# Optimization experiments

Measured on AMD Instinct MI355X. Metric: run time of the kernel, lower is better.

Reference implementation:

```python
import jax, jax.numpy as jnp
import numpy as np

N = 100000
D = 128      # embedding_dim
HID = 32     # hidden per head
HEADS = 4
OUT_C = 64
E = 1600000
NEG_SLOPE = 0.2


def setup_inputs() -> dict:
    key = jax.random.key(0)
    ks = jax.random.split(key, 12)
    inp = {}
    inp["x_indices"] = jnp.arange(N, dtype=jnp.int64)
    inp["ei"] = jax.random.randint(ks[0], (2, E), 0, N, dtype=jnp.int64)
    # parameters
    inp["emb"] = jax.random.normal(ks[1], (N, D), dtype=jnp.float32)
    # conv1: in=D, out=HID per head, HEADS heads, concat
    s1 = 1.0 / np.sqrt(D)
    inp["W1"] = jax.random.normal(ks[2], (D, HEADS * HID), dtype=jnp.float32) * s1
    inp["a_src1"] = jax.random.normal(ks[3], (HEADS, HID), dtype=jnp.float32) * s1
    inp["a_dst1"] = jax.random.normal(ks[4], (HEADS, HID), dtype=jnp.float32) * s1
    inp["b1"] = jnp.zeros((HEADS * HID,), dtype=jnp.float32)
    # conv2: in=HEADS*HID, out=OUT_C, 1 head
    s2 = 1.0 / np.sqrt(HEADS * HID)
    inp["W2"] = jax.random.normal(ks[5], (HEADS * HID, OUT_C), dtype=jnp.float32) * s2
    inp["a_src2"] = jax.random.normal(ks[6], (1, OUT_C), dtype=jnp.float32) * s2
    inp["a_dst2"] = jax.random.normal(ks[7], (1, OUT_C), dtype=jnp.float32) * s2
    inp["b2"] = jnp.zeros((OUT_C,), dtype=jnp.float32)
    return inp


def gat_conv(x, src, dst, W, a_src, a_dst, b, heads, out_ch, concat):
    # x: [N, Din]; src/dst: [E'] (self-loops already included)
    n = x.shape[0]
    h = (x @ W).reshape(n, heads, out_ch)          # [N, H, C]
    alpha_s = jnp.sum(h * a_src, axis=-1)          # [N, H]
    alpha_d = jnp.sum(h * a_dst, axis=-1)          # [N, H]
    e = alpha_s[src] + alpha_d[dst]                # [E', H]
    e = jnp.where(e > 0, e, NEG_SLOPE * e)         # leaky_relu
    # segment softmax over incoming edges per destination node
    m = jax.ops.segment_max(e, dst, num_segments=n)      # [N, H]
    ex = jnp.exp(e - m[dst])
    den = jax.ops.segment_sum(ex, dst, num_segments=n)   # [N, H]
    a = ex / den[dst]                              # [E', H]  (self-loops guarantee den>0)
    msg = h[src] * a[:, :, None]                   # [E', H, C]
    out = jax.ops.segment_sum(msg, dst, num_segments=n)  # [N, H, C]
    if concat:
        out = out.reshape(n, heads * out_ch)
    else:
        out = out.mean(axis=1)
    return out + b


def reference(x_indices, ei, emb, W1, a_src1, a_dst1, b1, W2, a_src2, a_dst2, b2):
    n = emb.shape[0]
    # PyG GATConv default add_self_loops=True
    loop = jnp.arange(n, dtype=ei.dtype)
    src = jnp.concatenate([ei[0], loop])
    dst = jnp.concatenate([ei[1], loop])
    x = emb[x_indices]                                  # embedding lookup
    x = jax.nn.elu(gat_conv(x, src, dst, W1, a_src1, a_dst1, b1, HEADS, HID, True))
    # dropout p=0.5 is identity in eval mode
    return gat_conv(x, src, dst, W2, a_src2, a_dst2, b2, 1, OUT_C, True)
```

## Files before the change

kernel.cpp:

```cpp
#include <hip/hip_runtime.h>
#include <math.h>

#define NEG_SLOPE 0.2f
#define BK_SHIFT 8

typedef __attribute__((ext_vector_type(2))) float v2f;

__device__ __forceinline__ float leaky(float x) { return x > 0.f ? x : NEG_SLOPE * x; }
__device__ __forceinline__ float dot4(float4 a, float4 b) {
    return a.x * b.x + a.y * b.y + a.z * b.z + a.w * b.w;
}
__device__ __forceinline__ unsigned short f2bf(float f) {
    unsigned int x = __float_as_uint(f);
    unsigned int r = (x + 0x7fffu + ((x >> 16) & 1u)) >> 16;
    return (unsigned short)r;
}
__device__ __forceinline__ float bflo(unsigned int u) { return __uint_as_float(u << 16); }
__device__ __forceinline__ float bfhi(unsigned int u) { return __uint_as_float(u & 0xffff0000u); }


__global__ void zero_kernel(int* __restrict__ p, int n) {
    int i = blockIdx.x * blockDim.x + threadIdx.x;
    if (i < n) p[i] = 0;
}

__global__ void __launch_bounds__(256) bcount_kernel(const int* __restrict__ ei, int E, int E2,
                                                     int K, int* __restrict__ bcounts) {
    __shared__ int h[512];
    int t = threadIdx.x;
    h[t] = 0; h[t + 256] = 0;
    __syncthreads();
    int base = blockIdx.x * 4096;
#pragma unroll 4
    for (int i = 0; i < 16; i++) {
        int e = base + i * 256 + t;
        if (e < E2) {
            int dst = (e < E) ? ei[E + e] : (e - E);
            atomicAdd(&h[dst >> BK_SHIFT], 1);
        }
    }
    __syncthreads();
    for (int b = t; b < K; b += 256) {
        int c = h[b];
        if (c) atomicAdd(&bcounts[b], c);
    }
}

__global__ void __launch_bounds__(512) bscan_kernel(const int* __restrict__ bcounts, int K,
                                                    int* __restrict__ bbase, int* __restrict__ bcursor) {
    __shared__ int s[512];
    int t = threadIdx.x;
    int v = (t < K) ? bcounts[t] : 0;
    s[t] = v;
    __syncthreads();
    for (int off = 1; off < 512; off <<= 1) {
        int u = (t >= off) ? s[t - off] : 0;
        __syncthreads();
        s[t] += u;
        __syncthreads();
    }
    if (t < K) {
        int ex = s[t] - v;
        bbase[t] = ex;
        bcursor[t] = ex;
    }
    if (t == 511) bbase[K] = s[511];
}

__global__ void __launch_bounds__(256) bscatter_kernel(const int* __restrict__ ei, int E, int E2,
                                                       int K, int* __restrict__ bcursor,
                                                       unsigned int* __restrict__ bedges) {
    __shared__ int hist[512], pre[512], lcur[512], gbase[512], psum[256];
    __shared__ unsigned int stage[4096];
    __shared__ unsigned short binof[4096];
    int t = threadIdx.x;
    hist[t] = 0; hist[t + 256] = 0;
    __syncthreads();
    int base = blockIdx.x * 4096;
    int cnt = min(4096, E2 - base);
    int s_[16], d_[16];
#pragma unroll
    for (int i = 0; i < 16; i++) {
        int e = base + i * 256 + t;
        if (e < E2) {
            int ss, dd;
            if (e < E) { ss = ei[e]; dd = ei[E + e]; }
            else       { ss = e - E; dd = ss; }
            s_[i] = ss; d_[i] = dd;
            atomicAdd(&hist[dd >> BK_SHIFT], 1);
        }
    }
    __syncthreads();
    int a0 = hist[2 * t], a1 = hist[2 * t + 1];
    psum[t] = a0 + a1;
    __syncthreads();
    for (int off = 1; off < 256; off <<= 1) {
        int u = (t >= off) ? psum[t - off] : 0;
        __syncthreads();
        psum[t] += u;
        __syncthreads();
    }
    int pex = psum[t] - (a0 + a1);
    pre[2 * t] = pex;
    pre[2 * t + 1] = pex + a0;
    __syncthreads();
    for (int b = t; b < K; b += 256) {
        int c = hist[b];
        if (c) gbase[b] = atomicAdd(&bcursor[b], c);
    }
    lcur[t] = pre[t]; lcur[t + 256] = pre[t + 256];
    __syncthreads();
#pragma unroll
    for (int i = 0; i < 16; i++) {
        int e = base + i * 256 + t;
        if (e < E2) {
            int bin = d_[i] >> BK_SHIFT;
            int p = atomicAdd(&lcur[bin], 1);
            stage[p] = ((unsigned)s_[i] << 8) | (unsigned)(d_[i] & 255);
            binof[p] = (unsigned short)bin;
        }
    }
    __syncthreads();
    for (int i = t; i < cnt; i += 256) {
        unsigned int ed = stage[i];
        int bin = (int)binof[i];
        bedges[gbase[bin] + (i - pre[bin])] = ed;
    }
}

__global__ void __launch_bounds__(256) bcsr_kernel(const unsigned int* __restrict__ bedges,
                                                   const int* __restrict__ bbase, int N,
                                                   int* __restrict__ counts, int* __restrict__ indptr,
                                                   int* __restrict__ csr) {
    __shared__ int hist[256], scn[256], cur[256];
    int b = blockIdx.x;
    int t = threadIdx.x;
    int base = bbase[b];
    int cnt = bbase[b + 1] - base;
    hist[t] = 0;
    __syncthreads();
    for (int i = t; i < cnt; i += 256) {
        atomicAdd(&hist[bedges[base + i] & 255u], 1);
    }
    __syncthreads();
    int v = hist[t];
    scn[t] = v;
    __syncthreads();
    for (int off = 1; off < 256; off <<= 1) {
        int u = (t >= off) ? scn[t - off] : 0;
        __syncthreads();
        scn[t] += u;
        __syncthreads();
    }
    int ex = scn[t] - v;
    int d = (b << BK_SHIFT) + t;
    if (d < N) { counts[d] = v; indptr[d] = base + ex; }
    cur[t] = ex;
    __syncthreads();
    for (int i = t; i < cnt; i += 256) {
        unsigned int ed = bedges[base + i];
        int p = atomicAdd(&cur[ed & 255u], 1);
        csr[base + p] = (int)(ed >> 8);
    }
}


__global__ __launch_bounds__(256) void gemm1_kernel(const float* __restrict__ emb,
                             const int* __restrict__ xidx,
                             const float* __restrict__ W1,
                             unsigned short* __restrict__ h1b,
                             const float* __restrict__ a_s1, const float* __restrict__ a_d1,
                             float* __restrict__ as1, float* __restrict__ ad1, int N) {
    __shared__ float xs[64][128];
    __shared__ float ws[128][64];
    int tid = threadIdx.x;
    int r0 = blockIdx.x * 64;
    int c0 = blockIdx.y * 64;
    {
        const float4* W4 = (const float4*)W1;
        float4* ws4 = (float4*)ws;
        int cbase = c0 >> 2;
        for (int i = tid; i < 128 * 16; i += 256) {
            int k = i >> 4, c = i & 15;
            ws4[i] = W4[k * 32 + cbase + c];
        }
    }
    {
        float4* xs4 = (float4*)xs;
        for (int i = tid; i < 64 * 32; i += 256) {
            int r = i >> 5, c = i & 31;
            int row = r0 + r;
            float4 v = make_float4(0.f, 0.f, 0.f, 0.f);
            if (row < N) {
                int s = xidx[row];
                v = ((const float4*)emb)[(size_t)s * 32 + c];
            }
            xs4[i] = v;
        }
    }
    __syncthreads();
    int tr = tid >> 4;
    int tc = tid & 15;
    float4 acc[4];
    acc[0] = acc[1] = acc[2] = acc[3] = make_float4(0.f, 0.f, 0.f, 0.f);
    for (int k = 0; k < 128; k += 4) {
        float4 wv0 = *(const float4*)&ws[k][tc * 4];
        float4 wv1 = *(const float4*)&ws[k + 1][tc * 4];
        float4 wv2 = *(const float4*)&ws[k + 2][tc * 4];
        float4 wv3 = *(const float4*)&ws[k + 3][tc * 4];
#pragma unroll
        for (int i = 0; i < 4; i++) {
            float4 xv = *(const float4*)&xs[tr * 4 + i][k];
            acc[i].x = fmaf(xv.x, wv0.x, acc[i].x);
            acc[i].y = fmaf(xv.x, wv0.y, acc[i].y);
            acc[i].z = fmaf(xv.x, wv0.z, acc[i].z);
            acc[i].w = fmaf(xv.x, wv0.w, acc[i].w);
            acc[i].x = fmaf(xv.y, wv1.x, acc[i].x);
            acc[i].y = fmaf(xv.y, wv1.y, acc[i].y);
            acc[i].z = fmaf(xv.y, wv1.z, acc[i].z);
            acc[i].w = fmaf(xv.y, wv1.w, acc[i].w);
            acc[i].x = fmaf(xv.z, wv2.x, acc[i].x);
            acc[i].y = fmaf(xv.z, wv2.y, acc[i].y);
            acc[i].z = fmaf(xv.z, wv2.z, acc[i].z);
            acc[i].w = fmaf(xv.z, wv2.w, acc[i].w);
            acc[i].x = fmaf(xv.w, wv3.x, acc[i].x);
            acc[i].y = fmaf(xv.w, wv3.y, acc[i].y);
            acc[i].z = fmaf(xv.w, wv3.z, acc[i].z);
            acc[i].w = fmaf(xv.w, wv3.w, acc[i].w);
        }
    }
    int colbase = c0 + tc * 4;
    int h = colbase >> 5;
    int off = colbase & 31;
    float4 av = *(const float4*)&a_s1[h * 32 + off];
    float4 dv = *(const float4*)&a_d1[h * 32 + off];
#pragma unroll
    for (int i = 0; i < 4; i++) {
        int row = r0 + tr * 4 + i;
        if (row < N) {
            ushort4 pk;
            pk.x = f2bf(acc[i].x); pk.y = f2bf(acc[i].y);
            pk.z = f2bf(acc[i].z); pk.w = f2bf(acc[i].w);
            *(ushort4*)&h1b[(size_t)row * 128 + colbase] = pk;
        }
        float ps = dot4(acc[i], av);
        float pd = dot4(acc[i], dv);
        ps += __shfl_xor(ps, 1); pd += __shfl_xor(pd, 1);
        ps += __shfl_xor(ps, 2); pd += __shfl_xor(pd, 2);
        ps += __shfl_xor(ps, 4); pd += __shfl_xor(pd, 4);
        if ((tc & 7) == 0 && row < N) {
            as1[row * 4 + h] = ps;
            ad1[row * 4 + h] = pd;
        }
    }
}


__global__ __launch_bounds__(256) void gemm2_kernel(const unsigned short* __restrict__ x1b,
                             const float* __restrict__ W2,
                             unsigned short* __restrict__ h2b,
                             const float* __restrict__ a_s2, const float* __restrict__ a_d2,
                             float* __restrict__ as2, float* __restrict__ ad2, int N) {
    __shared__ float xs[64][128];
    __shared__ float ws[128][64];
    int tid = threadIdx.x;
    int r0 = blockIdx.x * 64;
    {
        const float4* W4 = (const float4*)W2;
        float4* ws4 = (float4*)ws;
        for (int i = tid; i < 128 * 16; i += 256) ws4[i] = W4[i];
    }
    {
        const uint4* x4 = (const uint4*)x1b;
        for (int i = tid; i < 64 * 16; i += 256) {
            int r = i >> 4, c = i & 15;
            int row = r0 + r;
            uint4 u = make_uint4(0u, 0u, 0u, 0u);
            if (row < N) u = x4[(size_t)row * 16 + c];
            float* dst = &xs[r][c * 8];
            dst[0] = bflo(u.x); dst[1] = bfhi(u.x);
            dst[2] = bflo(u.y); dst[3] = bfhi(u.y);
            dst[4] = bflo(u.z); dst[5] = bfhi(u.z);
            dst[6] = bflo(u.w); dst[7] = bfhi(u.w);
        }
    }
    __syncthreads();
    int tr = tid >> 4;
    int tc = tid & 15;
    float4 acc[4];
    acc[0] = acc[1] = acc[2] = acc[3] = make_float4(0.f, 0.f, 0.f, 0.f);
    for (int k = 0; k < 128; k += 4) {
        float4 wv0 = *(const float4*)&ws[k][tc * 4];
        float4 wv1 = *(const float4*)&ws[k + 1][tc * 4];
        float4 wv2 = *(const float4*)&ws[k + 2][tc * 4];
        float4 wv3 = *(const float4*)&ws[k + 3][tc * 4];
#pragma unroll
        for (int i = 0; i < 4; i++) {
            float4 xv = *(const float4*)&xs[tr * 4 + i][k];
            acc[i].x = fmaf(xv.x, wv0.x, acc[i].x);
            acc[i].y = fmaf(xv.x, wv0.y, acc[i].y);
            acc[i].z = fmaf(xv.x, wv0.z, acc[i].z);
            acc[i].w = fmaf(xv.x, wv0.w, acc[i].w);
            acc[i].x = fmaf(xv.y, wv1.x, acc[i].x);
            acc[i].y = fmaf(xv.y, wv1.y, acc[i].y);
            acc[i].z = fmaf(xv.y, wv1.z, acc[i].z);
            acc[i].w = fmaf(xv.y, wv1.w, acc[i].w);
            acc[i].x = fmaf(xv.z, wv2.x, acc[i].x);
            acc[i].y = fmaf(xv.z, wv2.y, acc[i].y);
            acc[i].z = fmaf(xv.z, wv2.z, acc[i].z);
            acc[i].w = fmaf(xv.z, wv2.w, acc[i].w);
            acc[i].x = fmaf(xv.w, wv3.x, acc[i].x);
            acc[i].y = fmaf(xv.w, wv3.y, acc[i].y);
            acc[i].z = fmaf(xv.w, wv3.z, acc[i].z);
            acc[i].w = fmaf(xv.w, wv3.w, acc[i].w);
        }
    }
    float4 av = *(const float4*)&a_s2[tc * 4];
    float4 dv = *(const float4*)&a_d2[tc * 4];
#pragma unroll
    for (int i = 0; i < 4; i++) {
        int row = r0 + tr * 4 + i;
        if (row < N) {
            ushort4 pk;
            pk.x = f2bf(acc[i].x); pk.y = f2bf(acc[i].y);
            pk.z = f2bf(acc[i].z); pk.w = f2bf(acc[i].w);
            *(ushort4*)&h2b[(size_t)row * 64 + tc * 4] = pk;
        }
        float ps = dot4(acc[i], av);
        float pd = dot4(acc[i], dv);
        ps += __shfl_xor(ps, 1); pd += __shfl_xor(pd, 1);
        ps += __shfl_xor(ps, 2); pd += __shfl_xor(pd, 2);
        ps += __shfl_xor(ps, 4); pd += __shfl_xor(pd, 4);
        ps += __shfl_xor(ps, 8); pd += __shfl_xor(pd, 8);
        if (tc == 0 && row < N) { as2[row] = ps; ad2[row] = pd; }
    }
}


__device__ __forceinline__ void edge_fma(uint4 u0, float w, v2f* acc) {
    v2f wv = {w, w};
    v2f t;
    t.x = bflo(u0.x); t.y = bfhi(u0.x); acc[0] += wv * t;
    t.x = bflo(u0.y); t.y = bfhi(u0.y); acc[1] += wv * t;
    t.x = bflo(u0.z); t.y = bfhi(u0.z); acc[2] += wv * t;
    t.x = bflo(u0.w); t.y = bfhi(u0.w); acc[3] += wv * t;
}

__device__ __forceinline__ void accum_tbl1(int srcReg, const float* __restrict__ ew, int mcount,
                                           const uint4* __restrict__ h1v4,
                                           int lanebase, int sub, int cg, int hh, v2f* acc) {
    int b = 0;
    for (; b + 4 <= mcount; b += 4) {
        int i0 = b + sub, i1 = b + 2 + sub;
        int s0 = __shfl(srcReg, lanebase + i0);
        int s1 = __shfl(srcReg, lanebase + i1);
        float w_0 = ew[i0 * 4 + hh];
        float w_1 = ew[i1 * 4 + hh];
        uint4 u0 = h1v4[(unsigned)(s0 * 16 + cg)];
        uint4 u1 = h1v4[(unsigned)(s1 * 16 + cg)];
        edge_fma(u0, w_0, acc);
        edge_fma(u1, w_1, acc);
    }
    if (b + 2 <= mcount) {
        int i0 = b + sub;
        int s0 = __shfl(srcReg, lanebase + i0);
        float w_0 = ew[i0 * 4 + hh];
        uint4 u0 = h1v4[(unsigned)(s0 * 16 + cg)];
        edge_fma(u0, w_0, acc);
        b += 2;
    }
    if (b < mcount) {
        int s0 = __shfl(srcReg, lanebase + b);
        if (sub == 0) {
            float w_0 = ew[b * 4 + hh];
            uint4 u0 = h1v4[(unsigned)(s0 * 16 + cg)];
            edge_fma(u0, w_0, acc);
        }
    }
}

__global__ void __launch_bounds__(256)
agg1_kernel(const int* __restrict__ csr, const int* __restrict__ indptr,
            const int* __restrict__ counts, const float* __restrict__ as1,
            const float* __restrict__ ad1, const unsigned short* __restrict__ h1b,
            const float* __restrict__ b1, unsigned short* __restrict__ x1b, int N) {
    __shared__ float ewt[4][2][128];
    int lane = threadIdx.x & 63;
    int wv = threadIdx.x >> 6;
    int l32 = lane & 31;
    int lanebase = lane & 32;
    int n = blockIdx.x * 8 + wv * 2 + (lane >> 5);
    if (n >= N) return;
    int start = indptr[n];
    int cnt = counts[n];
    float4 ad4 = ((const float4*)ad1)[n];

    int src0 = 0;
    float4 p0 = make_float4(0.f, 0.f, 0.f, 0.f);
    if (l32 < cnt) {
        src0 = csr[start + l32];
        float4 a = ((const float4*)as1)[src0];
        p0.x = __expf(leaky(a.x + ad4.x));
        p0.y = __expf(leaky(a.y + ad4.y));
        p0.z = __expf(leaky(a.z + ad4.z));
        p0.w = __expf(leaky(a.w + ad4.w));
    }
    float4 l4 = p0;
    if (cnt > 32) {
        for (int base = 32; base < cnt; base += 32) {
            if (base + l32 < cnt) {
                int s = csr[start + base + l32];
                float4 a = ((const float4*)as1)[s];
                l4.x += __expf(leaky(a.x + ad4.x));
                l4.y += __expf(leaky(a.y + ad4.y));
                l4.z += __expf(leaky(a.z + ad4.z));
                l4.w += __expf(leaky(a.w + ad4.w));
            }
        }
    }
#pragma unroll
    for (int off = 16; off >= 1; off >>= 1) {
        l4.x += __shfl_xor(l4.x, off);
        l4.y += __shfl_xor(l4.y, off);
        l4.z += __shfl_xor(l4.z, off);
        l4.w += __shfl_xor(l4.w, off);
    }
    float4 li = make_float4(1.f / l4.x, 1.f / l4.y, 1.f / l4.z, 1.f / l4.w);
    float4 w0 = make_float4(p0.x * li.x, p0.y * li.y, p0.z * li.z, p0.w * li.w);

    float* ew = ewt[wv][lane >> 5];
    *(float4*)&ew[l32 * 4] = w0;

    int sub = l32 >> 4;
    int cg = lane & 15;
    int hh = cg >> 2;
    const uint4* h1v4 = (const uint4*)h1b;
    v2f acc[4];
    acc[0] = acc[1] = acc[2] = acc[3] = (v2f){0.f, 0.f};
    accum_tbl1(src0, ew, min(cnt, 32), h1v4, lanebase, sub, cg, hh, acc);
    if (cnt > 32) {
        for (int base = 32; base < cnt; base += 32) {
            int srcc = 0;
            float4 wc = make_float4(0.f, 0.f, 0.f, 0.f);
            if (base + l32 < cnt) {
                srcc = csr[start + base + l32];
                float4 a = ((const float4*)as1)[srcc];
                wc.x = __expf(leaky(a.x + ad4.x)) * li.x;
                wc.y = __expf(leaky(a.y + ad4.y)) * li.y;
                wc.z = __expf(leaky(a.z + ad4.z)) * li.z;
                wc.w = __expf(leaky(a.w + ad4.w)) * li.w;
            }
            *(float4*)&ew[l32 * 4] = wc;
            accum_tbl1(srcc, ew, min(cnt - base, 32), h1v4, lanebase, sub, cg, hh, acc);
        }
    }
#pragma unroll
    for (int i = 0; i < 4; i++) {
        acc[i].x += __shfl_xor(acc[i].x, 16);
        acc[i].y += __shfl_xor(acc[i].y, 16);
    }
    if (l32 < 16) {
        const float4* b4 = (const float4*)b1;
        float4 ba = b4[cg * 2], bb = b4[cg * 2 + 1];
        float o[8];
        o[0] = acc[0].x + ba.x; o[1] = acc[0].y + ba.y;
        o[2] = acc[1].x + ba.z; o[3] = acc[1].y + ba.w;
        o[4] = acc[2].x + bb.x; o[5] = acc[2].y + bb.y;
        o[6] = acc[3].x + bb.z; o[7] = acc[3].y + bb.w;
#pragma unroll
        for (int j = 0; j < 8; j++) o[j] = (o[j] > 0.f) ? o[j] : (__expf(o[j]) - 1.f);
        uint4 pk;
        pk.x = (unsigned)f2bf(o[0]) | ((unsigned)f2bf(o[1]) << 16);
        pk.y = (unsigned)f2bf(o[2]) | ((unsigned)f2bf(o[3]) << 16);
        pk.z = (unsigned)f2bf(o[4]) | ((unsigned)f2bf(o[5]) << 16);
        pk.w = (unsigned)f2bf(o[6]) | ((unsigned)f2bf(o[7]) << 16);
        *(uint4*)&x1b[(size_t)n * 128 + cg * 8] = pk;
    }
}


__device__ __forceinline__ void accum2(int srcReg, float wReg, int mcount,
                                       const uint4* __restrict__ h2v4,
                                       int lanebase, int sub, int cg, v2f* acc) {
    int b = 0;
    for (; b + 8 <= mcount; b += 8) {
        int i0 = b + sub, i1 = b + 4 + sub;
        int s0 = __shfl(srcReg, lanebase + i0);
        int s1 = __shfl(srcReg, lanebase + i1);
        float w_0 = __shfl(wReg, lanebase + i0);
        float w_1 = __shfl(wReg, lanebase + i1);
        uint4 u0 = h2v4[(unsigned)(s0 * 8 + cg)];
        uint4 u1 = h2v4[(unsigned)(s1 * 8 + cg)];
        edge_fma(u0, w_0, acc);
        edge_fma(u1, w_1, acc);
    }
    if (b + 4 <= mcount) {
        int i0 = b + sub;
        int s0 = __shfl(srcReg, lanebase + i0);
        float w_0 = __shfl(wReg, lanebase + i0);
        uint4 u0 = h2v4[(unsigned)(s0 * 8 + cg)];
        edge_fma(u0, w_0, acc);
        b += 4;
    }
    if (b < mcount) {
        int rem = mcount - b;
        int i0 = b + sub;
        int ic = min(i0, mcount - 1);
        int s0 = __shfl(srcReg, lanebase + ic);
        float w_0 = __shfl(wReg, lanebase + ic);
        if (sub < rem) {
            uint4 u0 = h2v4[(unsigned)(s0 * 8 + cg)];
            edge_fma(u0, w_0, acc);
        }
    }
}

__global__ void __launch_bounds__(256)
agg2_kernel(const int* __restrict__ csr, const int* __restrict__ indptr,
            const int* __restrict__ counts, const float* __restrict__ as2,
            const float* __restrict__ ad2, const unsigned short* __restrict__ h2b,
            const float* __restrict__ b2, float* __restrict__ out, int N) {
    int lane = threadIdx.x & 63;
    int l32 = lane & 31;
    int lanebase = lane & 32;
    int n = blockIdx.x * 8 + (threadIdx.x >> 6) * 2 + (lane >> 5);
    if (n >= N) return;
    int start = indptr[n];
    int cnt = counts[n];
    float ad = ad2[n];

    int src0 = 0;
    float p0 = 0.f;
    if (l32 < cnt) {
        src0 = csr[start + l32];
        p0 = __expf(leaky(as2[src0] + ad));
    }
    float l = p0;
    if (cnt > 32) {
        for (int base = 32; base < cnt; base += 32) {
            if (base + l32 < cnt)
                l += __expf(leaky(as2[csr[start + base + l32]] + ad));
        }
    }
#pragma unroll
    for (int off = 16; off >= 1; off >>= 1) l += __shfl_xor(l, off);
    float li = 1.f / l;
    float w0 = p0 * li;

    int sub = l32 >> 3;
    int cg = lane & 7;
    const uint4* h2v4 = (const uint4*)h2b;
    v2f acc[4];
    acc[0] = acc[1] = acc[2] = acc[3] = (v2f){0.f, 0.f};
    accum2(src0, w0, min(cnt, 32), h2v4, lanebase, sub, cg, acc);
    if (cnt > 32) {
        for (int base = 32; base < cnt; base += 32) {
            int srcc = 0;
            float wc = 0.f;
            if (base + l32 < cnt) {
                srcc = csr[start + base + l32];
                wc = __expf(leaky(as2[srcc] + ad)) * li;
            }
            accum2(srcc, wc, min(cnt - base, 32), h2v4, lanebase, sub, cg, acc);
        }
    }
#pragma unroll
    for (int i = 0; i < 4; i++) {
        acc[i].x += __shfl_xor(acc[i].x, 8);
        acc[i].x += __shfl_xor(acc[i].x, 16);
        acc[i].y += __shfl_xor(acc[i].y, 8);
        acc[i].y += __shfl_xor(acc[i].y, 16);
    }
    if (l32 < 8) {
        const float4* b4 = (const float4*)b2;
        float4 ba = b4[cg * 2], bb = b4[cg * 2 + 1];
        float4 o0, o1;
        o0.x = acc[0].x + ba.x; o0.y = acc[0].y + ba.y;
        o0.z = acc[1].x + ba.z; o0.w = acc[1].y + ba.w;
        o1.x = acc[2].x + bb.x; o1.y = acc[2].y + bb.y;
        o1.z = acc[3].x + bb.z; o1.w = acc[3].y + bb.w;
        float4* orow = (float4*)&out[(size_t)n * 64 + cg * 8];
        orow[0] = o0;
        orow[1] = o1;
    }
}


extern "C" void kernel_launch(void* const* d_in, const int* in_sizes, int n_in,
                              void* d_out, int out_size, void* d_ws, size_t ws_size,
                              hipStream_t stream) {
    const int*   xidx = (const int*)d_in[0];
    const int*   ei   = (const int*)d_in[1];
    const float* emb  = (const float*)d_in[2];
    const float* W1   = (const float*)d_in[3];
    const float* a_s1 = (const float*)d_in[4];
    const float* a_d1 = (const float*)d_in[5];
    const float* b1   = (const float*)d_in[6];
    const float* W2   = (const float*)d_in[7];
    const float* a_s2 = (const float*)d_in[8];
    const float* a_d2 = (const float*)d_in[9];
    const float* b2   = (const float*)d_in[10];
    float* out = (float*)d_out;

    const int N  = in_sizes[0];
    const int E  = in_sizes[1] / 2;
    const int E2 = E + N;
    const int K  = (N + 255) >> BK_SHIFT;

    int* ws_i    = (int*)d_ws;
    int* counts  = ws_i;
    int* indptr  = ws_i + N;
    int* bcounts = ws_i + 2 * (size_t)N;
    int* bbase   = ws_i + 2 * (size_t)N + 512;
    int* bcursor = ws_i + 2 * (size_t)N + 1032;
    int* csr     = ws_i + 2 * (size_t)N + 1544;
    size_t fbase = ((size_t)(2 * (size_t)N + 1544 + E2) + 3) & ~(size_t)3;
    float* ws_f = (float*)d_ws;
    unsigned short* h1b = (unsigned short*)(ws_f + fbase);
    unsigned short* x1b = (unsigned short*)(ws_f + fbase + (size_t)N * 64);
    float* as1 = ws_f + fbase + (size_t)N * 128;
    float* ad1 = as1 + (size_t)N * 4;
    unsigned short* h2b = h1b;
    float* as2 = as1;
    float* ad2 = ad1;
    unsigned int* bedges = (unsigned int*)x1b;

    int nchunks = (E2 + 4095) / 4096;
    zero_kernel<<<(K + 255) / 256, 256, 0, stream>>>(bcounts, K);
    bcount_kernel<<<nchunks, 256, 0, stream>>>(ei, E, E2, K, bcounts);
    bscan_kernel<<<1, 512, 0, stream>>>(bcounts, K, bbase, bcursor);
    bscatter_kernel<<<nchunks, 256, 0, stream>>>(ei, E, E2, K, bcursor, bedges);
    bcsr_kernel<<<K, 256, 0, stream>>>(bedges, bbase, N, counts, indptr, csr);

    {
        dim3 g((N + 63) / 64, 2);
        gemm1_kernel<<<g, 256, 0, stream>>>(emb, xidx, W1, h1b, a_s1, a_d1, as1, ad1, N);
    }
    agg1_kernel<<<(N + 7) / 8, 256, 0, stream>>>(csr, indptr, counts, as1, ad1, h1b, b1, x1b, N);

    gemm2_kernel<<<(N + 63) / 64, 256, 0, stream>>>(x1b, W2, h2b, a_s2, a_d2, as2, ad2, N);
    agg2_kernel<<<(N + 7) / 8, 256, 0, stream>>>(csr, indptr, counts, as2, ad2, h2b, b2, out, N);
}
```

Baseline: 424.1 us.

## Retile both GEMMs with K-split smaller shared tiles and unroll aggregation loops deeper

```diff
diff --git a/kernel.cpp b/kernel.cpp
--- a/kernel.cpp
+++ b/kernel.cpp
@@ -165,78 +165,82 @@
 }
 
 
+__device__ __forceinline__ void fma16(float4 xv, float4 wv0, float4 wv1,
+                                      float4 wv2, float4 wv3, float4& a) {
+    a.x = fmaf(xv.x, wv0.x, a.x); a.y = fmaf(xv.x, wv0.y, a.y);
+    a.z = fmaf(xv.x, wv0.z, a.z); a.w = fmaf(xv.x, wv0.w, a.w);
+    a.x = fmaf(xv.y, wv1.x, a.x); a.y = fmaf(xv.y, wv1.y, a.y);
+    a.z = fmaf(xv.y, wv1.z, a.z); a.w = fmaf(xv.y, wv1.w, a.w);
+    a.x = fmaf(xv.z, wv2.x, a.x); a.y = fmaf(xv.z, wv2.y, a.y);
+    a.z = fmaf(xv.z, wv2.z, a.z); a.w = fmaf(xv.z, wv2.w, a.w);
+    a.x = fmaf(xv.w, wv3.x, a.x); a.y = fmaf(xv.w, wv3.y, a.y);
+    a.z = fmaf(xv.w, wv3.z, a.z); a.w = fmaf(xv.w, wv3.w, a.w);
+}
+
+
 __global__ __launch_bounds__(256) void gemm1_kernel(const float* __restrict__ emb,
                              const int* __restrict__ xidx,
                              const float* __restrict__ W1,
                              unsigned short* __restrict__ h1b,
                              const float* __restrict__ a_s1, const float* __restrict__ a_d1,
                              float* __restrict__ as1, float* __restrict__ ad1, int N) {
-    __shared__ float xs[64][128];
-    __shared__ float ws[128][64];
+    __shared__ float xs[64][64];
+    __shared__ float ws[64][128];
     int tid = threadIdx.x;
     int r0 = blockIdx.x * 64;
-    int c0 = blockIdx.y * 64;
-    {
-        const float4* W4 = (const float4*)W1;
-        float4* ws4 = (float4*)ws;
-        int cbase = c0 >> 2;
-        for (int i = tid; i < 128 * 16; i += 256) {
-            int k = i >> 4, c = i & 15;
-            ws4[i] = W4[k * 32 + cbase + c];
-        }
-    }
-    {
-        float4* xs4 = (float4*)xs;
-        for (int i = tid; i < 64 * 32; i += 256) {
-            int r = i >> 5, c = i & 31;
+    int tr = tid >> 5;
+    int tc = tid & 31;
+    float4 acc[8];
+#pragma unroll
+    for (int i = 0; i < 8; i++) acc[i] = make_float4(0.f, 0.f, 0.f, 0.f);
+    const float4* W4 = (const float4*)W1;
+    const float4* emb4 = (const float4*)emb;
+    float4* ws4 = (float4*)ws;
+    float4* xs4 = (float4*)xs;
+
+    for (int half = 0; half < 2; half++) {
+        float4 wbuf[8];
+#pragma unroll
+        for (int j = 0; j < 8; j++) wbuf[j] = W4[half * 2048 + tid + j * 256];
+        float4 xbuf[4];
+#pragma unroll
+        for (int j = 0; j < 4; j++) {
+            int idx = tid + j * 256;
+            int r = idx >> 4, c = idx & 15;
             int row = r0 + r;
             float4 v = make_float4(0.f, 0.f, 0.f, 0.f);
             if (row < N) {
                 int s = xidx[row];
-                v = ((const float4*)emb)[(size_t)s * 32 + c];
+                v = emb4[(size_t)s * 32 + half * 16 + c];
             }
-            xs4[i] = v;
-        }
-    }
-    __syncthreads();
-    int tr = tid >> 4;
-    int tc = tid & 15;
-    float4 acc[4];
-    acc[0] = acc[1] = acc[2] = acc[3] = make_float4(0.f, 0.f, 0.f, 0.f);
-    for (int k = 0; k < 128; k += 4) {
-        float4 wv0 = *(const float4*)&ws[k][tc * 4];
-        float4 wv1 = *(const float4*)&ws[k + 1][tc * 4];
-        float4 wv2 = *(const float4*)&ws[k + 2][tc * 4];
-        float4 wv3 = *(const float4*)&ws[k + 3][tc * 4];
-#pragma unroll
-        for (int i = 0; i < 4; i++) {
-            float4 xv = *(const float4*)&xs[tr * 4 + i][k];
-            acc[i].x = fmaf(xv.x, wv0.x, acc[i].x);
-            acc[i].y = fmaf(xv.x, wv0.y, acc[i].y);
-            acc[i].z = fmaf(xv.x, wv0.z, acc[i].z);
-            acc[i].w = fmaf(xv.x, wv0.w, acc[i].w);
-            acc[i].x = fmaf(xv.y, wv1.x, acc[i].x);
-            acc[i].y = fmaf(xv.y, wv1.y, acc[i].y);
-            acc[i].z = fmaf(xv.y, wv1.z, acc[i].z);
-            acc[i].w = fmaf(xv.y, wv1.w, acc[i].w);
-            acc[i].x = fmaf(xv.z, wv2.x, acc[i].x);
-            acc[i].y = fmaf(xv.z, wv2.y, acc[i].y);
-            acc[i].z = fmaf(xv.z, wv2.z, acc[i].z);
-            acc[i].w = fmaf(xv.z, wv2.w, acc[i].w);
-            acc[i].x = fmaf(xv.w, wv3.x, acc[i].x);
-            acc[i].y = fmaf(xv.w, wv3.y, acc[i].y);
-            acc[i].z = fmaf(xv.w, wv3.z, acc[i].z);
-            acc[i].w = fmaf(xv.w, wv3.w, acc[i].w);
-        }
-    }
-    int colbase = c0 + tc * 4;
-    int h = colbase >> 5;
-    int off = colbase & 31;
+            xbuf[j] = v;
+        }
+        __syncthreads();
+#pragma unroll
+        for (int j = 0; j < 8; j++) ws4[tid + j * 256] = wbuf[j];
+#pragma unroll
+        for (int j = 0; j < 4; j++) xs4[tid + j * 256] = xbuf[j];
+        __syncthreads();
+        for (int k = 0; k < 64; k += 4) {
+            float4 wv0 = *(const float4*)&ws[k][tc * 4];
+            float4 wv1 = *(const float4*)&ws[k + 1][tc * 4];
+            float4 wv2 = *(const float4*)&ws[k + 2][tc * 4];
+            float4 wv3 = *(const float4*)&ws[k + 3][tc * 4];
+#pragma unroll
+            for (int i = 0; i < 8; i++) {
+                float4 xv = *(const float4*)&xs[tr * 8 + i][k];
+                fma16(xv, wv0, wv1, wv2, wv3, acc[i]);
+            }
+        }
+    }
+    int colbase = tc * 4;
+    int h = tc >> 3;
+    int off = (tc & 7) * 4;
     float4 av = *(const float4*)&a_s1[h * 32 + off];
     float4 dv = *(const float4*)&a_d1[h * 32 + off];
 #pragma unroll
-    for (int i = 0; i < 4; i++) {
-        int row = r0 + tr * 4 + i;
+    for (int i = 0; i < 8; i++) {
+        int row = r0 + tr * 8 + i;
         if (row < N) {
             ushort4 pk;
             pk.x = f2bf(acc[i].x); pk.y = f2bf(acc[i].y);
@@ -261,65 +265,64 @@
                              unsigned short* __restrict__ h2b,
                              const float* __restrict__ a_s2, const float* __restrict__ a_d2,
                              float* __restrict__ as2, float* __restrict__ ad2, int N) {
-    __shared__ float xs[64][128];
-    __shared__ float ws[128][64];
+    __shared__ float xs[128][68];
+    __shared__ float ws[64][64];
     int tid = threadIdx.x;
-    int r0 = blockIdx.x * 64;
-    {
-        const float4* W4 = (const float4*)W2;
-        float4* ws4 = (float4*)ws;
-        for (int i = tid; i < 128 * 16; i += 256) ws4[i] = W4[i];
-    }
-    {
-        const uint4* x4 = (const uint4*)x1b;
-        for (int i = tid; i < 64 * 16; i += 256) {
-            int r = i >> 4, c = i & 15;
+    int r0 = blockIdx.x * 128;
+    int tr = tid >> 4;
+    int tc = tid & 15;
+    float4 acc[8];
+#pragma unroll
+    for (int i = 0; i < 8; i++) acc[i] = make_float4(0.f, 0.f, 0.f, 0.f);
+    const float4* W4 = (const float4*)W2;
+    const uint4* x4 = (const uint4*)x1b;
+    float4* ws4 = (float4*)ws;
+
+    for (int half = 0; half < 2; half++) {
+        float4 wbuf[4];
+#pragma unroll
+        for (int j = 0; j < 4; j++) wbuf[j] = W4[half * 1024 + tid + j * 256];
+        uint4 xbuf[4];
+#pragma unroll
+        for (int j = 0; j < 4; j++) {
+            int idx = tid + j * 256;
+            int r = idx >> 3, c = idx & 7;
             int row = r0 + r;
             uint4 u = make_uint4(0u, 0u, 0u, 0u);
-            if (row < N) u = x4[(size_t)row * 16 + c];
-            float* dst = &xs[r][c * 8];
-            dst[0] = bflo(u.x); dst[1] = bfhi(u.x);
-            dst[2] = bflo(u.y); dst[3] = bfhi(u.y);
-            dst[4] = bflo(u.z); dst[5] = bfhi(u.z);
-            dst[6] = bflo(u.w); dst[7] = bfhi(u.w);
-        }
-    }
-    __syncthreads();
-    int tr = tid >> 4;
-    int tc = tid & 15;
-    float4 acc[4];
-    acc[0] = acc[1] = acc[2] = acc[3] = make_float4(0.f, 0.f, 0.f, 0.f);
-    for (int k = 0; k < 128; k += 4) {
-        float4 wv0 = *(const float4*)&ws[k][tc * 4];
-        float4 wv1 = *(const float4*)&ws[k + 1][tc * 4];
-        float4 wv2 = *(const float4*)&ws[k + 2][tc * 4];
-        float4 wv3 = *(const float4*)&ws[k + 3][tc * 4];
-#pragma unroll
-        for (int i = 0; i < 4; i++) {
-            float4 xv = *(const float4*)&xs[tr * 4 + i][k];
-            acc[i].x = fmaf(xv.x, wv0.x, acc[i].x);
-            acc[i].y = fmaf(xv.x, wv0.y, acc[i].y);
-            acc[i].z = fmaf(xv.x, wv0.z, acc[i].z);
-            acc[i].w = fmaf(xv.x, wv0.w, acc[i].w);
-            acc[i].x = fmaf(xv.y, wv1.x, acc[i].x);
-            acc[i].y = fmaf(xv.y, wv1.y, acc[i].y);
-            acc[i].z = fmaf(xv.y, wv1.z, acc[i].z);
-            acc[i].w = fmaf(xv.y, wv1.w, acc[i].w);
-            acc[i].x = fmaf(xv.z, wv2.x, acc[i].x);
-            acc[i].y = fmaf(xv.z, wv2.y, acc[i].y);
-            acc[i].z = fmaf(xv.z, wv2.z, acc[i].z);
-            acc[i].w = fmaf(xv.z, wv2.w, acc[i].w);
-            acc[i].x = fmaf(xv.w, wv3.x, acc[i].x);
-            acc[i].y = fmaf(xv.w, wv3.y, acc[i].y);
-            acc[i].z = fmaf(xv.w, wv3.z, acc[i].z);
-            acc[i].w = fmaf(xv.w, wv3.w, acc[i].w);
+            if (row < N) u = x4[(size_t)row * 16 + half * 8 + c];
+            xbuf[j] = u;
+        }
+        __syncthreads();
+#pragma unroll
+        for (int j = 0; j < 4; j++) ws4[tid + j * 256] = wbuf[j];
+#pragma unroll
+        for (int j = 0; j < 4; j++) {
+            int idx = tid + j * 256;
+            int r = idx >> 3, c = idx & 7;
+            uint4 u = xbuf[j];
+            float4 lo = make_float4(bflo(u.x), bfhi(u.x), bflo(u.y), bfhi(u.y));
+            float4 hi = make_float4(bflo(u.z), bfhi(u.z), bflo(u.w), bfhi(u.w));
+            *(float4*)&xs[r][c * 8] = lo;
+            *(float4*)&xs[r][c * 8 + 4] = hi;
+        }
+        __syncthreads();
+        for (int k = 0; k < 64; k += 4) {
+            float4 wv0 = *(const float4*)&ws[k][tc * 4];
+            float4 wv1 = *(const float4*)&ws[k + 1][tc * 4];
+            float4 wv2 = *(const float4*)&ws[k + 2][tc * 4];
+            float4 wv3 = *(const float4*)&ws[k + 3][tc * 4];
+#pragma unroll
+            for (int i = 0; i < 8; i++) {
+                float4 xv = *(const float4*)&xs[i * 16 + tr][k];
+                fma16(xv, wv0, wv1, wv2, wv3, acc[i]);
+            }
         }
     }
     float4 av = *(const float4*)&a_s2[tc * 4];
     float4 dv = *(const float4*)&a_d2[tc * 4];
 #pragma unroll
-    for (int i = 0; i < 4; i++) {
-        int row = r0 + tr * 4 + i;
+    for (int i = 0; i < 8; i++) {
+        int row = r0 + i * 16 + tr;
         if (row < N) {
             ushort4 pk;
             pk.x = f2bf(acc[i].x); pk.y = f2bf(acc[i].y);
@@ -350,7 +353,26 @@
                                            const uint4* __restrict__ h1v4,
                                            int lanebase, int sub, int cg, int hh, v2f* acc) {
     int b = 0;
-    for (; b + 4 <= mcount; b += 4) {
+    for (; b + 8 <= mcount; b += 8) {
+        int i0 = b + sub, i1 = b + 2 + sub, i2 = b + 4 + sub, i3 = b + 6 + sub;
+        int s0 = __shfl(srcReg, lanebase + i0);
+        int s1 = __shfl(srcReg, lanebase + i1);
+        int s2 = __shfl(srcReg, lanebase + i2);
+        int s3 = __shfl(srcReg, lanebase + i3);
+        float w_0 = ew[i0 * 4 + hh];
+        float w_1 = ew[i1 * 4 + hh];
+        float w_2 = ew[i2 * 4 + hh];
+        float w_3 = ew[i3 * 4 + hh];
+        uint4 u0 = h1v4[(unsigned)(s0 * 16 + cg)];
+        uint4 u1 = h1v4[(unsigned)(s1 * 16 + cg)];
+        uint4 u2 = h1v4[(unsigned)(s2 * 16 + cg)];
+        uint4 u3 = h1v4[(unsigned)(s3 * 16 + cg)];
+        edge_fma(u0, w_0, acc);
+        edge_fma(u1, w_1, acc);
+        edge_fma(u2, w_2, acc);
+        edge_fma(u3, w_3, acc);
+    }
+    if (b + 4 <= mcount) {
         int i0 = b + sub, i1 = b + 2 + sub;
         int s0 = __shfl(srcReg, lanebase + i0);
         int s1 = __shfl(srcReg, lanebase + i1);
@@ -360,6 +382,7 @@
         uint4 u1 = h1v4[(unsigned)(s1 * 16 + cg)];
         edge_fma(u0, w_0, acc);
         edge_fma(u1, w_1, acc);
+        b += 4;
     }
     if (b + 2 <= mcount) {
         int i0 = b + sub;
@@ -483,7 +506,26 @@
                                        const uint4* __restrict__ h2v4,
                                        int lanebase, int sub, int cg, v2f* acc) {
     int b = 0;
-    for (; b + 8 <= mcount; b += 8) {
+    for (; b + 16 <= mcount; b += 16) {
+        int i0 = b + sub, i1 = b + 4 + sub, i2 = b + 8 + sub, i3 = b + 12 + sub;
+        int s0 = __shfl(srcReg, lanebase + i0);
+        int s1 = __shfl(srcReg, lanebase + i1);
+        int s2 = __shfl(srcReg, lanebase + i2);
+        int s3 = __shfl(srcReg, lanebase + i3);
+        float w_0 = __shfl(wReg, lanebase + i0);
+        float w_1 = __shfl(wReg, lanebase + i1);
+        float w_2 = __shfl(wReg, lanebase + i2);
+        float w_3 = __shfl(wReg, lanebase + i3);
+        uint4 u0 = h2v4[(unsigned)(s0 * 8 + cg)];
+        uint4 u1 = h2v4[(unsigned)(s1 * 8 + cg)];
+        uint4 u2 = h2v4[(unsigned)(s2 * 8 + cg)];
+        uint4 u3 = h2v4[(unsigned)(s3 * 8 + cg)];
+        edge_fma(u0, w_0, acc);
+        edge_fma(u1, w_1, acc);
+        edge_fma(u2, w_2, acc);
+        edge_fma(u3, w_3, acc);
+    }
+    if (b + 8 <= mcount) {
         int i0 = b + sub, i1 = b + 4 + sub;
         int s0 = __shfl(srcReg, lanebase + i0);
         int s1 = __shfl(srcReg, lanebase + i1);
@@ -493,6 +535,7 @@
         uint4 u1 = h2v4[(unsigned)(s1 * 8 + cg)];
         edge_fma(u0, w_0, acc);
         edge_fma(u1, w_1, acc);
+        b += 8;
     }
     if (b + 4 <= mcount) {
         int i0 = b + sub;
@@ -632,12 +675,9 @@
     bscatter_kernel<<<nchunks, 256, 0, stream>>>(ei, E, E2, K, bcursor, bedges);
     bcsr_kernel<<<K, 256, 0, stream>>>(bedges, bbase, N, counts, indptr, csr);
 
-    {
-        dim3 g((N + 63) / 64, 2);
-        gemm1_kernel<<<g, 256, 0, stream>>>(emb, xidx, W1, h1b, a_s1, a_d1, as1, ad1, N);
-    }
+    gemm1_kernel<<<(N + 63) / 64, 256, 0, stream>>>(emb, xidx, W1, h1b, a_s1, a_d1, as1, ad1, N);
     agg1_kernel<<<(N + 7) / 8, 256, 0, stream>>>(csr, indptr, counts, as1, ad1, h1b, b1, x1b, N);
 
-    gemm2_kernel<<<(N + 63) / 64, 256, 0, stream>>>(x1b, W2, h2b, a_s2, a_d2, as2, ad2, N);
+    gemm2_kernel<<<(N + 127) / 128, 256, 0, stream>>>(x1b, W2, h2b, a_s2, a_d2, as2, ad2, N);
     agg2_kernel<<<(N + 7) / 8, 256, 0, stream>>>(csr, indptr, counts, as2, ad2, h2b, b2, out, N);
 }
```

Measured after the change: 427.3 us. About the same (+0.7%).
